# Performance work log

Hardware: AMD Instinct MI355X
Metric: run time of the kernel (lower is better)

Reference implementation:

```python
import jax, jax.numpy as jnp
import numpy as np

N_NODES = 100000
N_EDGES = 3200000
D_FEAT = 128
K_ADJ = 3


def setup_inputs() -> dict:
    key = jax.random.key(0)
    k1, k2, k3, k4 = jax.random.split(key, 4)
    x = jax.random.normal(k1, (N_NODES, D_FEAT), dtype=jnp.float32)
    adj_rows = jax.random.randint(k2, (K_ADJ, N_EDGES), 0, N_NODES, dtype=jnp.int32)
    adj_cols = jax.random.randint(k3, (K_ADJ, N_EDGES), 0, N_NODES, dtype=jnp.int32)
    adj_vals = jax.random.uniform(k4, (K_ADJ, N_EDGES), dtype=jnp.float32)
    return {"x": x, "adj_rows": adj_rows, "adj_cols": adj_cols, "adj_vals": adj_vals, "idx": 1}


def reference(x, adj_rows, adj_cols, adj_vals, idx):
    # torch.spmm(adjs[idx], x): out[r] = sum_{e: rows[e]==r} vals[e] * x[cols[e]]
    rows = adj_rows[idx]
    cols = adj_cols[idx]
    vals = adj_vals[idx]
    gathered = x[cols] * vals[:, None]  # [nnz, F]
    out = jax.ops.segment_sum(gathered, rows, num_segments=N_NODES)  # [N, F]
    return out
```

## Files before the change

kernel.cpp:

```cpp
#include <hip/hip_runtime.h>

#define N_NODES 100000
#define N_EDGES 3200000
#define D_FEAT  128

#define RPB 128
#define NB ((N_NODES + RPB - 1) / RPB)
#define P3_THREADS 512
#define P3_EPT 16
#define P3_TILE (P3_THREADS * P3_EPT)
#define P3_GRID ((N_EDGES + P3_TILE - 1) / P3_TILE)

#define NS 25
#define NCELL (RPB * NS)
#define CAP 4608

#define CVT_BLOCKS 2048
#define HIST_BLOCKS 256


__device__ inline unsigned bf16rne(float f) {
    unsigned u = __float_as_uint(f);
    u += 0x7fffu + ((u >> 16) & 1u);
    return u >> 16;
}
__device__ inline unsigned pack2(float lo, float hi) {
    return bf16rne(lo) | (bf16rne(hi) << 16);
}

__global__ __launch_bounds__(256) void cvt_bhist_kernel(
    const float* __restrict__ x, uint4* __restrict__ xb,
    const int* __restrict__ adj_rows, const int* __restrict__ idx_p,
    int* __restrict__ bhist)
{
    __shared__ int lh[NB];
    if (blockIdx.x < CVT_BLOCKS) {
        const int total = N_NODES * D_FEAT / 8;
        for (int i = blockIdx.x * 256 + threadIdx.x; i < total;
             i += CVT_BLOCKS * 256) {
            const float4 a = reinterpret_cast<const float4*>(x)[2 * i];
            const float4 b = reinterpret_cast<const float4*>(x)[2 * i + 1];
            uint4 o;
            o.x = pack2(a.x, a.y);
            o.y = pack2(a.z, a.w);
            o.z = pack2(b.x, b.y);
            o.w = pack2(b.z, b.w);
            xb[i] = o;
        }
    } else {
        for (int i = threadIdx.x; i < NB; i += 256) lh[i] = 0;
        __syncthreads();
        const long long idx = (long long)idx_p[0];
        const int* rows = adj_rows + idx * (long long)N_EDGES;
        for (int e = (blockIdx.x - CVT_BLOCKS) * 256 + threadIdx.x;
             e < N_EDGES; e += HIST_BLOCKS * 256)
            atomicAdd(&lh[rows[e] >> 7], 1);
        __syncthreads();
        for (int i = threadIdx.x; i < NB; i += 256)
            if (lh[i]) atomicAdd(&bhist[i], lh[i]);
    }
}

__global__ __launch_bounds__(1024) void bscan_kernel(
    const int* __restrict__ bhist, int* __restrict__ bptr,
    int* __restrict__ bcursor)
{
    __shared__ int lds[1024];
    const int t = threadIdx.x;
    const int v = (t < NB) ? bhist[t] : 0;
    lds[t] = v;
    __syncthreads();
    for (int off = 1; off < 1024; off <<= 1) {
        int u = (t >= off) ? lds[t - off] : 0;
        __syncthreads();
        lds[t] += u;
        __syncthreads();
    }
    if (t < NB) {
        const int excl = lds[t] - v;
        bptr[t]    = excl;
        bcursor[t] = excl;
    }
    if (t == NB - 1) bptr[NB] = lds[t];
}

__global__ __launch_bounds__(P3_THREADS) void partition_kernel(
    const int* __restrict__ adj_rows, const int* __restrict__ adj_cols,
    const float* __restrict__ adj_vals, const int* __restrict__ idx_p,
    int* __restrict__ bcursor, int2* __restrict__ pairs)
{
    __shared__ int lcnt[NB];
    __shared__ int lbase[NB];
    const long long idx = (long long)idx_p[0];
    const int*   rows = adj_rows + idx * (long long)N_EDGES;
    const int*   cols = adj_cols + idx * (long long)N_EDGES;
    const float* vals = adj_vals + idx * (long long)N_EDGES;

    const int tile = blockIdx.x * P3_TILE;
    for (int i = threadIdx.x; i < NB; i += P3_THREADS) lcnt[i] = 0;
    __syncthreads();

    for (int k = 0; k < P3_EPT; ++k) {
        const int e = tile + k * P3_THREADS + (int)threadIdx.x;
        if (e < N_EDGES) atomicAdd(&lcnt[rows[e] >> 7], 1);
    }
    __syncthreads();

    for (int i = threadIdx.x; i < NB; i += P3_THREADS) {
        const int c = lcnt[i];
        lbase[i] = c ? atomicAdd(&bcursor[i], c) : 0;
        lcnt[i]  = 0;
    }
    __syncthreads();

    for (int k = 0; k < P3_EPT; ++k) {
        const int e = tile + k * P3_THREADS + (int)threadIdx.x;
        if (e < N_EDGES) {
            const int r = rows[e];
            const int b = r >> 7;
            const int pos = lbase[b] + atomicAdd(&lcnt[b], 1);
            pairs[pos] = make_int2(((r & (RPB - 1)) << 24) | cols[e],
                                   __float_as_int(vals[e]));
        }
    }
}

__global__ __launch_bounds__(1024) void sort_spmm_kernel(
    const uint4* __restrict__ xb, const int* __restrict__ bptr,
    const int2* __restrict__ pairs, float* __restrict__ out)
{
    __shared__ int2 staged[CAP];
    __shared__ int  cellptr[NCELL];
    __shared__ int  rs[RPB + 1];
    __shared__ int  scan[1024];
    const int b    = blockIdx.x;
    const int t    = (int)threadIdx.x;
    const int base = bptr[b];
    const int n    = bptr[b + 1] - base;

    for (int i = t; i < NCELL; i += 1024) cellptr[i] = 0;
    __syncthreads();

    for (int i = t; i < n; i += 1024) {
        const int2 p = pairs[base + i];
        const int row = ((unsigned)p.x) >> 24;
        const int col = p.x & 0xFFFFFF;
        atomicAdd(&cellptr[row * NS + (col >> 12)], 1);
    }
    __syncthreads();

    const int i0 = t * 4;
    int v0 = 0, v1 = 0, v2 = 0, v3 = 0;
    if (i0 + 0 < NCELL) v0 = cellptr[i0 + 0];
    if (i0 + 1 < NCELL) v1 = cellptr[i0 + 1];
    if (i0 + 2 < NCELL) v2 = cellptr[i0 + 2];
    if (i0 + 3 < NCELL) v3 = cellptr[i0 + 3];
    const int s = v0 + v1 + v2 + v3;
    scan[t] = s;
    __syncthreads();
    for (int off = 1; off < 1024; off <<= 1) {
        int u = (t >= off) ? scan[t - off] : 0;
        __syncthreads();
        scan[t] += u;
        __syncthreads();
    }
    int run = scan[t] - s;
    if (i0 + 0 < NCELL) { cellptr[i0 + 0] = run; run += v0; }
    if (i0 + 1 < NCELL) { cellptr[i0 + 1] = run; run += v1; }
    if (i0 + 2 < NCELL) { cellptr[i0 + 2] = run; run += v2; }
    if (i0 + 3 < NCELL) { cellptr[i0 + 3] = run; run += v3; }
    __syncthreads();

    if (t < RPB) rs[t] = cellptr[t * NS];
    if (t == 0)  rs[RPB] = n;
    __syncthreads();

    for (int i = t; i < n; i += 1024) {
        const int2 p = pairs[base + i];
        const int row = ((unsigned)p.x) >> 24;
        const int col = p.x & 0xFFFFFF;
        const int pos = atomicAdd(&cellptr[row * NS + (col >> 12)], 1);
        if (pos < CAP) staged[pos] = p;
    }
    __syncthreads();

    const int w    = t >> 6;
    const int lane = t & 63;
    const int g    = lane >> 4;
    const int sl   = lane & 15;
    const int grp  = w * 4 + g;

    for (int k = 0; k < 2; ++k) {
        const int r   = grp + 64 * k;
        const int row = b * RPB + r;
        if (row >= N_NODES) break;
        const int s0 = rs[r];
        const int e0 = rs[r + 1];

        float4 a0 = make_float4(0.f, 0.f, 0.f, 0.f);
        float4 a1 = make_float4(0.f, 0.f, 0.f, 0.f);
        for (int j = s0; j < e0; ++j) {
            const int2  p   = staged[j];
            const int   col = p.x & 0xFFFFFF;
            const float vj  = __int_as_float(p.y);
            const uint4 wv  = xb[(size_t)col * (D_FEAT / 8) + sl];
            a0.x += vj * __uint_as_float(wv.x << 16);
            a0.y += vj * __uint_as_float(wv.x & 0xffff0000u);
            a0.z += vj * __uint_as_float(wv.y << 16);
            a0.w += vj * __uint_as_float(wv.y & 0xffff0000u);
            a1.x += vj * __uint_as_float(wv.z << 16);
            a1.y += vj * __uint_as_float(wv.z & 0xffff0000u);
            a1.z += vj * __uint_as_float(wv.w << 16);
            a1.w += vj * __uint_as_float(wv.w & 0xffff0000u);
        }
        float* op = out + (size_t)row * D_FEAT + sl * 8;
        *reinterpret_cast<float4*>(op)     = a0;
        *reinterpret_cast<float4*>(op + 4) = a1;
    }
}

__global__ __launch_bounds__(256) void spmm_atomic_kernel(
    const float* __restrict__ x,
    const int*   __restrict__ adj_rows,
    const int*   __restrict__ adj_cols,
    const float* __restrict__ adj_vals,
    const int*   __restrict__ idx_p,
    float*       __restrict__ out)
{
    const long long idx = (long long)idx_p[0];
    const int*   rows = adj_rows + idx * (long long)N_EDGES;
    const int*   cols = adj_cols + idx * (long long)N_EDGES;
    const float* vals = adj_vals + idx * (long long)N_EDGES;

    long long tt = (long long)blockIdx.x * blockDim.x + threadIdx.x;
    long long e  = tt >> 5;
    int       f4 = (int)(tt & 31);
    if (e >= N_EDGES) return;

    const int   r = rows[e];
    const int   c = cols[e];
    const float v = vals[e];
    const float4 xv =
        *reinterpret_cast<const float4*>(x + (long long)c * D_FEAT + f4 * 4);
    float* o = out + (long long)r * D_FEAT + f4 * 4;
    unsafeAtomicAdd(o + 0, v * xv.x);
    unsafeAtomicAdd(o + 1, v * xv.y);
    unsafeAtomicAdd(o + 2, v * xv.z);
    unsafeAtomicAdd(o + 3, v * xv.w);
}

extern "C" void kernel_launch(void* const* d_in, const int* in_sizes, int n_in,
                              void* d_out, int out_size, void* d_ws, size_t ws_size,
                              hipStream_t stream) {
    const float* x        = (const float*)d_in[0];
    const int*   adj_rows = (const int*)  d_in[1];
    const int*   adj_cols = (const int*)  d_in[2];
    const float* adj_vals = (const float*)d_in[3];
    const int*   idx_p    = (const int*)  d_in[4];
    float*       out      = (float*)d_out;

    const size_t n_meta_raw = (size_t)NB * 3 + 1;
    const size_t n_meta     = (n_meta_raw + 3) & ~(size_t)3;
    const size_t need       = (n_meta + (size_t)2 * N_EDGES) * 4
                            + (size_t)N_NODES * D_FEAT * 2;

    if (ws_size < need) {
        hipMemsetAsync(out, 0, (size_t)out_size * sizeof(float), stream);
        const long long total_threads = (long long)N_EDGES * 32;
        const int block = 256;
        const long long grid = (total_threads + block - 1) / block;
        spmm_atomic_kernel<<<(dim3)(unsigned)grid, block, 0, stream>>>(
            x, adj_rows, adj_cols, adj_vals, idx_p, out);
        return;
    }

    int*   bhist   = (int*)d_ws;
    int*   bptr    = bhist + NB;
    int*   bcursor = bptr + (NB + 1);
    int2*  pairs   = (int2*)((int*)d_ws + n_meta);
    uint4* xb      = (uint4*)((int*)d_ws + n_meta + (size_t)2 * N_EDGES);

    hipMemsetAsync(bhist, 0, (size_t)NB * sizeof(int), stream);

    cvt_bhist_kernel<<<CVT_BLOCKS + HIST_BLOCKS, 256, 0, stream>>>(
        x, xb, adj_rows, idx_p, bhist);
    bscan_kernel<<<1, 1024, 0, stream>>>(bhist, bptr, bcursor);
    partition_kernel<<<P3_GRID, P3_THREADS, 0, stream>>>(
        adj_rows, adj_cols, adj_vals, idx_p, bcursor, pairs);
    sort_spmm_kernel<<<NB, 1024, 0, stream>>>(xb, bptr, pairs, out);
}
```

Before: 232.7 us.

## Precompute per-cell histogram in histogram pass to skip counting pass in sort kernel

The histogram kernel now also builds a global per-(row, column-bucket) count array using global atomics. The sort kernel reads these counts directly instead of re-reading all pairs and counting in shared memory. The partition kernel keeps row indices in registers so they are loaded once instead of twice, and the histogram block count is doubled. The cost is a larger memset (about 12.8 MB of cell counts) and millions of scattered global atomics in the histogram pass.

```diff
diff --git a/kernel.cpp b/kernel.cpp
--- a/kernel.cpp
+++ b/kernel.cpp
@@ -13,10 +13,11 @@
 
 #define NS 25
 #define NCELL (RPB * NS)
+#define NCELLG ((size_t)NB * RPB * NS)
 #define CAP 4608
 
 #define CVT_BLOCKS 2048
-#define HIST_BLOCKS 256
+#define HIST_BLOCKS 512
 
 
 __device__ inline unsigned bf16rne(float f) {
@@ -30,8 +31,9 @@
 
 __global__ __launch_bounds__(256) void cvt_bhist_kernel(
     const float* __restrict__ x, uint4* __restrict__ xb,
-    const int* __restrict__ adj_rows, const int* __restrict__ idx_p,
-    int* __restrict__ bhist)
+    const int* __restrict__ adj_rows, const int* __restrict__ adj_cols,
+    const int* __restrict__ idx_p,
+    int* __restrict__ bhist, int* __restrict__ cellhist)
 {
     __shared__ int lh[NB];
     if (blockIdx.x < CVT_BLOCKS) {
@@ -52,9 +54,14 @@
         __syncthreads();
         const long long idx = (long long)idx_p[0];
         const int* rows = adj_rows + idx * (long long)N_EDGES;
+        const int* cols = adj_cols + idx * (long long)N_EDGES;
         for (int e = (blockIdx.x - CVT_BLOCKS) * 256 + threadIdx.x;
-             e < N_EDGES; e += HIST_BLOCKS * 256)
-            atomicAdd(&lh[rows[e] >> 7], 1);
+             e < N_EDGES; e += HIST_BLOCKS * 256) {
+            const int r = rows[e];
+            atomicAdd(&lh[r >> 7], 1);
+            if (cellhist)
+                atomicAdd(&cellhist[(size_t)r * NS + (cols[e] >> 12)], 1);
+        }
         __syncthreads();
         for (int i = threadIdx.x; i < NB; i += 256)
             if (lh[i]) atomicAdd(&bhist[i], lh[i]);
@@ -100,9 +107,12 @@
     for (int i = threadIdx.x; i < NB; i += P3_THREADS) lcnt[i] = 0;
     __syncthreads();
 
+    int rc[P3_EPT];
+#pragma unroll
     for (int k = 0; k < P3_EPT; ++k) {
         const int e = tile + k * P3_THREADS + (int)threadIdx.x;
-        if (e < N_EDGES) atomicAdd(&lcnt[rows[e] >> 7], 1);
+        rc[k] = (e < N_EDGES) ? rows[e] : -1;
+        if (rc[k] >= 0) atomicAdd(&lcnt[rc[k] >> 7], 1);
     }
     __syncthreads();
 
@@ -113,10 +123,11 @@
     }
     __syncthreads();
 
+#pragma unroll
     for (int k = 0; k < P3_EPT; ++k) {
-        const int e = tile + k * P3_THREADS + (int)threadIdx.x;
-        if (e < N_EDGES) {
-            const int r = rows[e];
+        const int r = rc[k];
+        if (r >= 0) {
+            const int e = tile + k * P3_THREADS + (int)threadIdx.x;
             const int b = r >> 7;
             const int pos = lbase[b] + atomicAdd(&lcnt[b], 1);
             pairs[pos] = make_int2(((r & (RPB - 1)) << 24) | cols[e],
@@ -125,9 +136,11 @@
     }
 }
 
+template <bool PRE>
 __global__ __launch_bounds__(1024) void sort_spmm_kernel(
     const uint4* __restrict__ xb, const int* __restrict__ bptr,
-    const int2* __restrict__ pairs, float* __restrict__ out)
+    const int2* __restrict__ pairs, const int* __restrict__ cellhist,
+    float* __restrict__ out)
 {
     __shared__ int2 staged[CAP];
     __shared__ int  cellptr[NCELL];
@@ -138,23 +151,32 @@
     const int base = bptr[b];
     const int n    = bptr[b + 1] - base;
 
-    for (int i = t; i < NCELL; i += 1024) cellptr[i] = 0;
-    __syncthreads();
-
-    for (int i = t; i < n; i += 1024) {
-        const int2 p = pairs[base + i];
-        const int row = ((unsigned)p.x) >> 24;
-        const int col = p.x & 0xFFFFFF;
-        atomicAdd(&cellptr[row * NS + (col >> 12)], 1);
-    }
-    __syncthreads();
-
     const int i0 = t * 4;
     int v0 = 0, v1 = 0, v2 = 0, v3 = 0;
-    if (i0 + 0 < NCELL) v0 = cellptr[i0 + 0];
-    if (i0 + 1 < NCELL) v1 = cellptr[i0 + 1];
-    if (i0 + 2 < NCELL) v2 = cellptr[i0 + 2];
-    if (i0 + 3 < NCELL) v3 = cellptr[i0 + 3];
+
+    if constexpr (PRE) {
+        const int* cb = cellhist + (size_t)b * NCELL;
+        if (i0 + 0 < NCELL) v0 = cb[i0 + 0];
+        if (i0 + 1 < NCELL) v1 = cb[i0 + 1];
+        if (i0 + 2 < NCELL) v2 = cb[i0 + 2];
+        if (i0 + 3 < NCELL) v3 = cb[i0 + 3];
+    } else {
+        for (int i = t; i < NCELL; i += 1024) cellptr[i] = 0;
+        __syncthreads();
+        for (int i = t; i < n; i += 1024) {
+            const int2 p = pairs[base + i];
+            const int row = ((unsigned)p.x) >> 24;
+            const int col = p.x & 0xFFFFFF;
+            atomicAdd(&cellptr[row * NS + (col >> 12)], 1);
+        }
+        __syncthreads();
+        if (i0 + 0 < NCELL) v0 = cellptr[i0 + 0];
+        if (i0 + 1 < NCELL) v1 = cellptr[i0 + 1];
+        if (i0 + 2 < NCELL) v2 = cellptr[i0 + 2];
+        if (i0 + 3 < NCELL) v3 = cellptr[i0 + 3];
+        __syncthreads();
+    }
+
     const int s = v0 + v1 + v2 + v3;
     scan[t] = s;
     __syncthreads();
@@ -261,10 +283,11 @@
 
     const size_t n_meta_raw = (size_t)NB * 3 + 1;
     const size_t n_meta     = (n_meta_raw + 3) & ~(size_t)3;
-    const size_t need       = (n_meta + (size_t)2 * N_EDGES) * 4
-                            + (size_t)N_NODES * D_FEAT * 2;
-
-    if (ws_size < need) {
+    const size_t xb_bytes   = (size_t)N_NODES * D_FEAT * 2;
+    const size_t need_pre   = (n_meta + NCELLG + (size_t)2 * N_EDGES) * 4 + xb_bytes;
+    const size_t need_base  = (n_meta + (size_t)2 * N_EDGES) * 4 + xb_bytes;
+
+    if (ws_size < need_base) {
         hipMemsetAsync(out, 0, (size_t)out_size * sizeof(float), stream);
         const long long total_threads = (long long)N_EDGES * 32;
         const int block = 256;
@@ -274,18 +297,28 @@
         return;
     }
 
-    int*   bhist   = (int*)d_ws;
-    int*   bptr    = bhist + NB;
-    int*   bcursor = bptr + (NB + 1);
-    int2*  pairs   = (int2*)((int*)d_ws + n_meta);
-    uint4* xb      = (uint4*)((int*)d_ws + n_meta + (size_t)2 * N_EDGES);
-
-    hipMemsetAsync(bhist, 0, (size_t)NB * sizeof(int), stream);
+    const bool pre = (ws_size >= need_pre);
+
+    int*   bhist    = (int*)d_ws;
+    int*   bptr     = bhist + NB;
+    int*   bcursor  = bptr + (NB + 1);
+    int*   cellhist = pre ? ((int*)d_ws + n_meta) : nullptr;
+    int*   after    = (int*)d_ws + n_meta + (pre ? NCELLG : 0);
+    int2*  pairs    = (int2*)after;
+    uint4* xb       = (uint4*)(after + (size_t)2 * N_EDGES);
+
+    hipMemsetAsync(d_ws, 0,
+                   (n_meta + (pre ? NCELLG : 0)) * sizeof(int), stream);
 
     cvt_bhist_kernel<<<CVT_BLOCKS + HIST_BLOCKS, 256, 0, stream>>>(
-        x, xb, adj_rows, idx_p, bhist);
+        x, xb, adj_rows, adj_cols, idx_p, bhist, cellhist);
     bscan_kernel<<<1, 1024, 0, stream>>>(bhist, bptr, bcursor);
     partition_kernel<<<P3_GRID, P3_THREADS, 0, stream>>>(
         adj_rows, adj_cols, adj_vals, idx_p, bcursor, pairs);
-    sort_spmm_kernel<<<NB, 1024, 0, stream>>>(xb, bptr, pairs, out);
-}
+    if (pre)
+        sort_spmm_kernel<true><<<NB, 1024, 0, stream>>>(
+            xb, bptr, pairs, cellhist, out);
+    else
+        sort_spmm_kernel<false><<<NB, 1024, 0, stream>>>(
+            xb, bptr, pairs, nullptr, out);
+}
```

Result: slower. 345.1 us (+48.3%).
